# Optimization experiments

Hardware: AMD Instinct MI355X
Metric: run time of the kernel (lower is better)

The kernel has to match this reference:

```python
import jax, jax.numpy as jnp
import numpy as np

B, T, L = 32, 256, 784          # batch, decode steps, context length (H*W)
H, E, V = 512, 256, 8000        # decoder hidden, embedding dim, vocab


def setup_inputs() -> dict:
    key = jax.random.key(0)
    ks = jax.random.split(key, 8)
    s = 0.02
    return {
        "cnn_feats": jax.random.normal(ks[0], (B, L, H), jnp.float32),
        "seq": jax.random.randint(ks[1], (B, T), 0, V),
        "embed_w": jax.random.normal(ks[2], (V, E), jnp.float32) * s,
        "w_ih": jax.random.normal(ks[3], (4 * H, E + H), jnp.float32) * s,
        "w_hh": jax.random.normal(ks[4], (4 * H, H), jnp.float32) * s,
        "w_hm": jax.random.normal(ks[5], (H, H), jnp.float32) * s,
        "w_out": jax.random.normal(ks[6], (H, 2 * H), jnp.float32) * s,
        "w_logit": jax.random.normal(ks[7], (V, H), jnp.float32) * s,
        "b_logit": jnp.zeros((V,), jnp.float32),
    }


def reference(cnn_feats, seq, embed_w, w_ih, w_hh, w_hm, w_out, w_logit, b_logit):
    # embed = Embedding -> ReLU (dropout is identity in eval / p=0)
    xs = jax.nn.relu(embed_w[seq])                      # [B, T, E]
    z = jnp.zeros((B, H), cnn_feats.dtype)

    def step(carry, xt):
        h, c, ctx_out = carry
        # LSTMCell (bias=False), input = concat([xt, prev context_output])
        inp = jnp.concatenate([xt, ctx_out], axis=-1)   # [B, E+H]
        gates = inp @ w_ih.T + h @ w_hh.T               # [B, 4H]
        i, f, g, o = jnp.split(gates, 4, axis=-1)       # torch gate order i,f,g,o
        c = jax.nn.sigmoid(f) * c + jax.nn.sigmoid(i) * jnp.tanh(g)
        h = jax.nn.sigmoid(o) * jnp.tanh(c)
        # dot-product attention over context
        mapped = h @ w_hm.T                             # [B, H]
        attn = jax.nn.softmax(jnp.einsum('blh,bh->bl', cnn_feats, mapped), axis=-1)
        ctx = jnp.einsum('bl,blh->bh', attn, cnn_feats)  # [B, H]
        out = jnp.tanh(jnp.concatenate([ctx, h], axis=-1) @ w_out.T)  # [B, H]
        logp = jax.nn.log_softmax(out @ w_logit.T + b_logit, axis=-1)  # [B, V]
        return (h, c, out), logp

    _, logps = jax.lax.scan(step, (z, z, z), jnp.swapaxes(xs, 0, 1))
    return jnp.swapaxes(logps, 0, 1)                    # [B, T, V]
```

## Files before the change

kernel.cpp:

```cpp
#include <hip/hip_runtime.h>
#include <hip/hip_bf16.h>
#include <stdint.h>

typedef unsigned short u16;
typedef unsigned int u32;
typedef unsigned long long u64;
typedef __attribute__((ext_vector_type(8))) short s16x8;
typedef __attribute__((ext_vector_type(4))) float f32x4;

#define AGT __HIP_MEMORY_SCOPE_AGENT

static __device__ __forceinline__ float bf2f(u16 u){
  unsigned v = ((unsigned)u) << 16; return __builtin_bit_cast(float, v);
}
static __device__ __forceinline__ u16 f2bf(float f){
  unsigned u = __builtin_bit_cast(unsigned, f);
  u += 0x7FFFu + ((u >> 16) & 1u);
  return (u16)(u >> 16);
}
static __device__ __forceinline__ float sigm(float x){ return 1.f / (1.f + __expf(-x)); }

typedef __attribute__((address_space(1))) const u32 gu32;
typedef __attribute__((address_space(3))) u32 lu32;
static __device__ __forceinline__ void gload_lds16(const void* g, void* l){
  __builtin_amdgcn_global_load_lds((gu32*)g, (lu32*)l, 16, 0, 0);
}

static __device__ __forceinline__ u64 tload(const u64* p){
  return __hip_atomic_load(p, __ATOMIC_RELAXED, AGT);
}
static __device__ __forceinline__ void tstore(u64* p, u64 v){
  __hip_atomic_store(p, v, __ATOMIC_RELAXED, AGT);
}
static __device__ __forceinline__ u32 wtag(u64 v){ return (u32)(v >> 32); }
static __device__ __forceinline__ s16x8 pack4(u64 q0, u64 q1, u64 q2, u64 q3){
  u32 a0=(u32)q0, a1=(u32)q1, a2=(u32)q2, a3=(u32)q3;
  s16x8 r = {(short)a0,(short)(a0>>16),(short)a1,(short)(a1>>16),
             (short)a2,(short)(a2>>16),(short)a3,(short)(a3>>16)};
  return r;
}


__global__ __launch_bounds__(256) void k_wfull(const float* __restrict__ wih,
                                               const float* __restrict__ whh,
                                               u16* __restrict__ wf){
  int stride = gridDim.x * blockDim.x;
  for (int i = blockIdx.x * blockDim.x + threadIdx.x; i < 2048 * 1280; i += stride){
    int j = i / 1280, k = i - j * 1280;
    float v = (k < 768) ? wih[j * 768 + k] : whh[j * 512 + (k - 768)];
    wf[i] = f2bf(v);
  }
}

__global__ __launch_bounds__(256) void k_whmt(const float* __restrict__ whm,
                                              u16* __restrict__ wt){
  int stride = gridDim.x * blockDim.x;
  for (int i = blockIdx.x * blockDim.x + threadIdx.x; i < 512 * 512; i += stride){
    int n = i >> 9, k = i & 511;
    wt[i] = f2bf(whm[k * 512 + n]);
  }
}

__global__ __launch_bounds__(256) void k_cvt(const float* __restrict__ s,
                                             u16* __restrict__ d, int n){
  int stride = gridDim.x * blockDim.x * 4;
  for (int i = (blockIdx.x * blockDim.x + threadIdx.x) * 4; i < n; i += stride){
    float4 v = *(const float4*)&s[i];
    d[i + 0] = f2bf(v.x); d[i + 1] = f2bf(v.y);
    d[i + 2] = f2bf(v.z); d[i + 3] = f2bf(v.w);
  }
}

__global__ __launch_bounds__(256) void k_xs(const int* __restrict__ seq,
                                            const float* __restrict__ emb,
                                            u16* __restrict__ xs){
  int stride = gridDim.x * blockDim.x;
  for (int i = blockIdx.x * blockDim.x + threadIdx.x; i < 8192 * 256; i += stride){
    int m = i >> 8, e = i & 255;
    int b = m >> 8, t = m & 255;
    float v = emb[(size_t)seq[m] * 256 + e];
    xs[(size_t)(t * 32 + b) * 256 + e] = f2bf(v > 0.f ? v : 0.f);
  }
}


template<int OUTBF, int HASBIAS, int NG>
__global__ __launch_bounds__(256) void k_gemm(const u16* __restrict__ A,
                                              const u16* __restrict__ Bm,
                                              void* __restrict__ Cout,
                                              const float* __restrict__ bias,
                                              int M, int N, int K){
  __shared__ __align__(16) u16 As[128 * 64];
  __shared__ __align__(16) u16 Bs[128 * 64];
  int tid = threadIdx.x; int w = tid >> 6; int l = tid & 63;
  int m0 = blockIdx.x * 128, n0 = blockIdx.y * 128;
  int wr = w >> 1, wc = w & 1;
  f32x4 acc[4][4];
#pragma unroll
  for (int a = 0; a < 4; a++)
#pragma unroll
    for (int b = 0; b < 4; b++){ f32x4 z = {0.f,0.f,0.f,0.f}; acc[a][b] = z; }
  int rA = m0 + (tid >> 3);
  int rB = n0 + (tid >> 3);
  for (int k0 = 0; k0 < K; k0 += 64){
    __syncthreads();
    int ca = k0 + (tid & 7) * 8;
#pragma unroll
    for (int i = 0; i < 4; i++){
      gload_lds16(&A[(size_t)(rA + i * 32) * K + ca], &As[i * 2048 + w * 512]);
      int rb = rB + i * 32;
      if (NG) rb = (rb < N - 1) ? rb : (N - 1);
      gload_lds16(&Bm[(size_t)rb * K + ca], &Bs[i * 2048 + w * 512]);
    }
    asm volatile("s_waitcnt vmcnt(0)" ::: "memory");
    __syncthreads();
#pragma unroll
    for (int ks = 0; ks < 2; ks++){
      s16x8 av[4], bv[4];
      int ko = ks * 32 + (l >> 4) * 8;
#pragma unroll
      for (int i = 0; i < 4; i++) av[i] = *(const s16x8*)&As[(wr * 64 + i * 16 + (l & 15)) * 64 + ko];
#pragma unroll
      for (int i = 0; i < 4; i++) bv[i] = *(const s16x8*)&Bs[(wc * 64 + i * 16 + (l & 15)) * 64 + ko];
#pragma unroll
      for (int mi = 0; mi < 4; mi++)
#pragma unroll
        for (int ni = 0; ni < 4; ni++)
          acc[mi][ni] = __builtin_amdgcn_mfma_f32_16x16x32_bf16(av[mi], bv[ni], acc[mi][ni], 0, 0, 0);
    }
  }
#pragma unroll
  for (int mi = 0; mi < 4; mi++)
#pragma unroll
    for (int ni = 0; ni < 4; ni++){
      int row = m0 + wr * 64 + mi * 16 + (l >> 4) * 4;
      int col = n0 + wc * 64 + ni * 16 + (l & 15);
      if (NG && col >= N) continue;
#pragma unroll
      for (int r = 0; r < 4; r++){
        float v = acc[mi][ni][r];
        if (HASBIAS) v += bias[col];
        if (OUTBF) ((u16*)Cout)[(size_t)(row + r) * N + col] = f2bf(v);
        else       ((float*)Cout)[(size_t)(row + r) * N + col] = v;
      }
    }
}


static __device__ void gates_role(const u16* __restrict__ WF, const u16* __restrict__ XS,
                                  u64* __restrict__ ZH, u64* __restrict__ ZO,
                                  float* __restrict__ CST, float* __restrict__ SM, int g){
  const int tid = threadIdx.x, w = tid >> 6, l = tid & 63;
  const int ns = g << 4;
  float (*red)[32][64] = (float(*)[32][64])SM;

  s16x8 bx[2][4], bh[4][4], bo[4][4];
#pragma unroll
  for (int ki = 0; ki < 2; ki++){
    int ko = w * 64 + ki * 32 + (l >> 4) * 8;
#pragma unroll
    for (int gi = 0; gi < 4; gi++)
      bx[ki][gi] = *(const s16x8*)&WF[(size_t)(gi * 512 + ns + (l & 15)) * 1280 + ko];
  }
#pragma unroll
  for (int ki = 0; ki < 4; ki++){
    int koh = 768 + w * 128 + ki * 32 + (l >> 4) * 8;
    int koo = 256 + w * 128 + ki * 32 + (l >> 4) * 8;
#pragma unroll
    for (int gi = 0; gi < 4; gi++){
      bh[ki][gi] = *(const s16x8*)&WF[(size_t)(gi * 512 + ns + (l & 15)) * 1280 + koh];
      bo[ki][gi] = *(const s16x8*)&WF[(size_t)(gi * 512 + ns + (l & 15)) * 1280 + koo];
    }
  }

  for (int t = 0; t < 256; ++t){
    const u32 tg = (u32)t;
    const int rp = (t + 1) & 1;
    f32x4 acc[2][4];
#pragma unroll
    for (int a = 0; a < 2; a++)
#pragma unroll
      for (int b = 0; b < 4; b++){ f32x4 z = {0.f,0.f,0.f,0.f}; acc[a][b] = z; }

#pragma unroll
    for (int ki = 0; ki < 2; ki++){
      int ko = w * 64 + ki * 32 + (l >> 4) * 8;
      s16x8 av[2];
#pragma unroll
      for (int mi = 0; mi < 2; mi++)
        av[mi] = *(const s16x8*)&XS[(size_t)(t * 32 + mi * 16 + (l & 15)) * 256 + ko];
#pragma unroll
      for (int mi = 0; mi < 2; mi++)
#pragma unroll
        for (int gi = 0; gi < 4; gi++)
          acc[mi][gi] = __builtin_amdgcn_mfma_f32_16x16x32_bf16(av[mi], bx[ki][gi], acc[mi][gi], 0, 0, 0);
    }
    if (t > 0){
#pragma unroll
      for (int kk = 0; kk < 4; kk++){
        int wb = w * 64 + kk * 16 + ((l >> 4) << 2);
        const u64* p0 = &ZH[(size_t)rp * 8192 + (size_t)(l & 15) * 256 + wb];
        const u64* p1 = &ZH[(size_t)rp * 8192 + (size_t)(16 + (l & 15)) * 256 + wb];
        u64 qa0,qa1,qa2,qa3,qb0,qb1,qb2,qb3; bool ok;
        do {
          qa0=tload(p0); qa1=tload(p0+1); qa2=tload(p0+2); qa3=tload(p0+3);
          qb0=tload(p1); qb1=tload(p1+1); qb2=tload(p1+2); qb3=tload(p1+3);
          ok = (wtag(qa0)==tg)&(wtag(qa1)==tg)&(wtag(qa2)==tg)&(wtag(qa3)==tg)
             & (wtag(qb0)==tg)&(wtag(qb1)==tg)&(wtag(qb2)==tg)&(wtag(qb3)==tg);
          if (!ok) __builtin_amdgcn_s_sleep(1);
        } while (!__all(ok));
        s16x8 av0 = pack4(qa0,qa1,qa2,qa3), av1 = pack4(qb0,qb1,qb2,qb3);
#pragma unroll
        for (int gi = 0; gi < 4; gi++){
          acc[0][gi] = __builtin_amdgcn_mfma_f32_16x16x32_bf16(av0, bh[kk][gi], acc[0][gi], 0, 0, 0);
          acc[1][gi] = __builtin_amdgcn_mfma_f32_16x16x32_bf16(av1, bh[kk][gi], acc[1][gi], 0, 0, 0);
        }
      }
#pragma unroll
      for (int kk = 0; kk < 4; kk++){
        int wb = w * 64 + kk * 16 + ((l >> 4) << 2);
        const u64* p0 = &ZO[(size_t)rp * 8192 + (size_t)(l & 15) * 256 + wb];
        const u64* p1 = &ZO[(size_t)rp * 8192 + (size_t)(16 + (l & 15)) * 256 + wb];
        u64 qa0,qa1,qa2,qa3,qb0,qb1,qb2,qb3; bool ok;
        do {
          qa0=tload(p0); qa1=tload(p0+1); qa2=tload(p0+2); qa3=tload(p0+3);
          qb0=tload(p1); qb1=tload(p1+1); qb2=tload(p1+2); qb3=tload(p1+3);
          ok = (wtag(qa0)==tg)&(wtag(qa1)==tg)&(wtag(qa2)==tg)&(wtag(qa3)==tg)
             & (wtag(qb0)==tg)&(wtag(qb1)==tg)&(wtag(qb2)==tg)&(wtag(qb3)==tg);
          if (!ok) __builtin_amdgcn_s_sleep(1);
        } while (!__all(ok));
        s16x8 av0 = pack4(qa0,qa1,qa2,qa3), av1 = pack4(qb0,qb1,qb2,qb3);
#pragma unroll
        for (int gi = 0; gi < 4; gi++){
          acc[0][gi] = __builtin_amdgcn_mfma_f32_16x16x32_bf16(av0, bo[kk][gi], acc[0][gi], 0, 0, 0);
          acc[1][gi] = __builtin_amdgcn_mfma_f32_16x16x32_bf16(av1, bo[kk][gi], acc[1][gi], 0, 0, 0);
        }
      }
    }
#pragma unroll
    for (int mi = 0; mi < 2; mi++)
#pragma unroll
      for (int gi = 0; gi < 4; gi++)
#pragma unroll
        for (int r = 0; r < 4; r++)
          red[w][mi * 16 + (l >> 4) * 4 + r][gi * 16 + (l & 15)] = acc[mi][gi][r];
    __syncthreads();
    {
      int bi = tid >> 3, j = (tid & 7) * 2;
      float iv0=0,fv0=0,gv0=0,ov0=0, iv1=0,fv1=0,gv1=0,ov1=0;
#pragma unroll
      for (int qq = 0; qq < 4; qq++){
        iv0 += red[qq][bi][j];      fv0 += red[qq][bi][16 + j];
        gv0 += red[qq][bi][32 + j]; ov0 += red[qq][bi][48 + j];
        iv1 += red[qq][bi][j + 1];      fv1 += red[qq][bi][16 + j + 1];
        gv1 += red[qq][bi][32 + j + 1]; ov1 += red[qq][bi][48 + j + 1];
      }
      int n0 = ns + j;
      float c0 = (t > 0) ? CST[bi * 512 + n0]     : 0.f;
      float c1 = (t > 0) ? CST[bi * 512 + n0 + 1] : 0.f;
      float cn0 = sigm(fv0) * c0 + sigm(iv0) * tanhf(gv0);
      float cn1 = sigm(fv1) * c1 + sigm(iv1) * tanhf(gv1);
      float h0 = sigm(ov0) * tanhf(cn0);
      float h1 = sigm(ov1) * tanhf(cn1);
      CST[bi * 512 + n0] = cn0; CST[bi * 512 + n0 + 1] = cn1;
      u32 pk = (u32)f2bf(h0) | ((u32)f2bf(h1) << 16);
      tstore(&ZH[(size_t)(t & 1) * 8192 + (size_t)bi * 256 + g * 8 + (tid & 7)],
             ((u64)(u32)(t + 1) << 32) | pk);
    }
    __syncthreads();
  }
}


static __device__ void attn_role(const u16* __restrict__ CNN2, const u16* __restrict__ CNNB,
                                 const u16* __restrict__ WOUT,
                                 u64* __restrict__ ZH, u64* __restrict__ ZO,
                                 u64* __restrict__ UT, u64* __restrict__ MST,
                                 u16* __restrict__ OALL, float* __restrict__ SM, int q){
  const int tid = threadIdx.x, w = tid >> 6, l = tid & 63;
  const int b = q / 7, ch = q - b * 7;
  const int l0 = ch * 112;
  const int nc = (ch == 6) ? 68 : 74, cs = ch * 74;
  u16*   hsh  = (u16*)SM;
  u16*   pbf  = (u16*)(SM + 256);
  float* sc   = SM + 320;
  float* scp  = SM + 448;
  float* msh  = SM + 896;
  u32*   zsh  = (u32*)(SM + 912);
  float* opart= SM + 1424;

  s16x8 a2[7][4];
  s16x8 vb[8][4];
#pragma unroll
  for (int tile = 0; tile < 7; tile++)
#pragma unroll
    for (int kk = 0; kk < 4; kk++)
      a2[tile][kk] = *(const s16x8*)&CNN2[(size_t)(b * 784 + l0 + tile * 16 + (l & 15)) * 512
                                          + w * 128 + kk * 32 + (l >> 4) * 8];
#pragma unroll
  for (int nt = 0; nt < 8; nt++)
#pragma unroll
    for (int kk = 0; kk < 4; kk++){
      int col = w * 128 + nt * 16 + (l & 15);
#pragma unroll
      for (int j = 0; j < 8; j++){
        int krow = kk * 32 + (l >> 4) * 8 + j;
        vb[nt][kk][j] = (krow < 112)
          ? (short)CNNB[(size_t)(b * 784 + l0 + krow) * 512 + col] : (short)0;
      }
    }

  for (int t = 0; t < 256; ++t){
    const u32 tagp = (u32)(t + 1);
    if (w == 0){
      const u64* hp = &ZH[(size_t)(t & 1) * 8192 + (size_t)b * 256 + l * 4];
      u64 h0,h1,h2,h3; bool ok;
      do {
        h0=tload(hp); h1=tload(hp+1); h2=tload(hp+2); h3=tload(hp+3);
        ok = (wtag(h0)==tagp)&(wtag(h1)==tagp)&(wtag(h2)==tagp)&(wtag(h3)==tagp);
        if (!ok) __builtin_amdgcn_s_sleep(1);
      } while (!__all(ok));
      *(s16x8*)&hsh[l * 8] = pack4(h0,h1,h2,h3);
    }
    __syncthreads();

    f32x4 sac[7];
#pragma unroll
    for (int tile = 0; tile < 7; tile++){ f32x4 z = {0.f,0.f,0.f,0.f}; sac[tile] = z; }
#pragma unroll
    for (int kk = 0; kk < 4; kk++){
      s16x8 bv = *(const s16x8*)&hsh[w * 128 + kk * 32 + (l >> 4) * 8];
#pragma unroll
      for (int tile = 0; tile < 7; tile++)
        sac[tile] = __builtin_amdgcn_mfma_f32_16x16x32_bf16(a2[tile][kk], bv, sac[tile], 0, 0, 0);
    }
    if ((l & 15) == 0){
#pragma unroll
      for (int tile = 0; tile < 7; tile++)
#pragma unroll
        for (int r = 0; r < 4; r++)
          scp[w * 112 + tile * 16 + (l >> 4) * 4 + r] = sac[tile][r];
    }
    __syncthreads();
    if (tid < 112) sc[tid] = scp[tid] + scp[112 + tid] + scp[224 + tid] + scp[336 + tid];
    else if (tid < 128) sc[tid] = -1e30f;
    __syncthreads();
    float m2 = fmaxf(sc[l], sc[l + 64]);
#pragma unroll
    for (int mk = 1; mk < 64; mk <<= 1) m2 = fmaxf(m2, __shfl_xor(m2, mk, 64));
    float M = m2;
    __syncthreads();
    if (tid < 112){ float p = __expf(sc[tid] - M); sc[tid] = p; pbf[tid] = f2bf(p); }
    else if (tid < 128){ sc[tid] = 0.f; pbf[tid] = 0; }
    __syncthreads();
    float s2 = sc[l] + sc[l + 64];
#pragma unroll
    for (int mk = 1; mk < 64; mk <<= 1) s2 += __shfl_xor(s2, mk, 64);
    float S = s2;

    f32x4 uac[8];
#pragma unroll
    for (int nt = 0; nt < 8; nt++){ f32x4 z = {0.f,0.f,0.f,0.f}; uac[nt] = z; }
#pragma unroll
    for (int kk = 0; kk < 4; kk++){
      s16x8 av = *(const s16x8*)&pbf[kk * 32 + (l >> 4) * 8];
#pragma unroll
      for (int nt = 0; nt < 8; nt++)
        uac[nt] = __builtin_amdgcn_mfma_f32_16x16x32_bf16(av, vb[nt][kk], uac[nt], 0, 0, 0);
    }
#pragma unroll
    for (int nt = 0; nt < 8; nt++){
      float o0 = uac[nt][0];
      float o1 = __shfl_xor(o0, 1, 64);
      if (l < 16 && (l & 1) == 0){
        u64 wv = ((u64)tagp << 32) | (u32)f2bf(o0) | ((u32)f2bf(o1) << 16);
        tstore(&UT[((size_t)(b * 7 + ch)) * 256 + w * 64 + nt * 8 + (l >> 1)], wv);
      }
    }
    if (tid == 0){
      tstore(&MST[(b * 7 + ch) * 2 + 0], ((u64)tagp << 32) | __builtin_bit_cast(u32, M));
      tstore(&MST[(b * 7 + ch) * 2 + 1], ((u64)tagp << 32) | __builtin_bit_cast(u32, S));
    }

    if (w == 0){
      const u64* mp_ = &MST[(b * 7) * 2 + ((l < 14) ? l : 0)];
      u64 v; bool ok;
      do {
        v = tload(mp_);
        ok = (wtag(v) == tagp);
        if (!ok) __builtin_amdgcn_s_sleep(1);
      } while (!__all(ok));
      if (l < 14) msh[l] = __builtin_bit_cast(float, (u32)v);
    }
    __syncthreads();
    float Mg = -1e30f;
#pragma unroll
    for (int c = 0; c < 7; c++) Mg = fmaxf(Mg, msh[2 * c]);
    float bet[7]; float Sg = 0.f;
#pragma unroll
    for (int c = 0; c < 7; c++){
      float e = __expf(msh[2 * c] - Mg);
      bet[c] = e; Sg += e * msh[2 * c + 1];
    }
    float inv = 1.f / Sg;
    {
      u64 uw[7]; bool ok;
      do {
#pragma unroll
        for (int c = 0; c < 7; c++) uw[c] = tload(&UT[((size_t)(b * 7 + c)) * 256 + tid]);
        ok = true;
#pragma unroll
        for (int c = 0; c < 7; c++) ok &= (wtag(uw[c]) == tagp);
        if (!ok) __builtin_amdgcn_s_sleep(1);
      } while (!__all(ok));
      float c0 = 0.f, c1 = 0.f;
#pragma unroll
      for (int c = 0; c < 7; c++){
        float bc = bet[c] * inv;
        c0 = fmaf(bc, bf2f((u16)uw[c]), c0);
        c1 = fmaf(bc, bf2f((u16)(uw[c] >> 16)), c1);
      }
      zsh[tid] = (u32)f2bf(c0) | ((u32)f2bf(c1) << 16);
      zsh[256 + tid] = ((u32*)hsh)[tid];
    }
    __syncthreads();

    f32x4 oac[5];
#pragma unroll
    for (int tile = 0; tile < 5; tile++){ f32x4 z = {0.f,0.f,0.f,0.f}; oac[tile] = z; }
#pragma unroll
    for (int kk = 0; kk < 8; kk++){
      int ko = w * 256 + kk * 32 + (l >> 4) * 8;
      s16x8 bv = *(const s16x8*)((const u16*)zsh + ko);
#pragma unroll
      for (int tile = 0; tile < 5; tile++){
        int row = cs + tile * 16 + (l & 15);
        row = (row < 511) ? row : 511;
        s16x8 av = *(const s16x8*)&WOUT[(size_t)row * 1024 + ko];
        oac[tile] = __builtin_amdgcn_mfma_f32_16x16x32_bf16(av, bv, oac[tile], 0, 0, 0);
      }
    }
    if ((l & 15) == 0){
#pragma unroll
      for (int tile = 0; tile < 5; tile++)
#pragma unroll
        for (int r = 0; r < 4; r++)
          opart[w * 80 + tile * 16 + (l >> 4) * 4 + r] = oac[tile][r];
    }
    __syncthreads();
    if (tid < (nc >> 1)){
      int j0 = 2 * tid;
      float v0 = opart[j0]   + opart[80 + j0]   + opart[160 + j0]   + opart[240 + j0];
      float v1 = opart[j0+1] + opart[80 + j0+1] + opart[160 + j0+1] + opart[240 + j0+1];
      u32 pk = (u32)f2bf(tanhf(v0)) | ((u32)f2bf(tanhf(v1)) << 16);
      tstore(&ZO[(size_t)(t & 1) * 8192 + (size_t)b * 256 + (cs >> 1) + tid],
             ((u64)tagp << 32) | pk);
      *(u32*)&OALL[((size_t)(b * 256 + t)) * 512 + cs + j0] = pk;
    }
    __syncthreads();
  }
}


__global__ __launch_bounds__(256, 1) void k_persist(const u16* __restrict__ WF,
                                                    const u16* __restrict__ XS,
                                                    const u16* __restrict__ CNN2,
                                                    const u16* __restrict__ CNNB,
                                                    const u16* __restrict__ WOUT,
                                                    u64* __restrict__ ZH,
                                                    u64* __restrict__ ZO,
                                                    u64* __restrict__ UT,
                                                    u64* __restrict__ MST,
                                                    float* __restrict__ CST,
                                                    u16* __restrict__ OALL){
  __shared__ __align__(16) float SM[8192];
  int gid = blockIdx.x;
  if (gid < 32)
    gates_role(WF, XS, ZH, ZO, CST, SM, gid);
  else
    attn_role(CNN2, CNNB, WOUT, ZH, ZO, UT, MST, OALL, SM, gid - 32);
}


__global__ __launch_bounds__(256) void k_lsm(float* __restrict__ x){
  size_t base = (size_t)blockIdx.x * 8000;
  int tid = threadIdx.x, w = tid >> 6, ln = tid & 63;
  __shared__ float sred[4];
  float m = -1e30f;
  for (int v = tid; v < 8000; v += 256) m = fmaxf(m, x[base + v]);
#pragma unroll
  for (int mk = 1; mk < 64; mk <<= 1) m = fmaxf(m, __shfl_xor(m, mk, 64));
  if (ln == 0) sred[w] = m;
  __syncthreads();
  float M = fmaxf(fmaxf(sred[0], sred[1]), fmaxf(sred[2], sred[3]));
  __syncthreads();
  float s = 0.f;
  for (int v = tid; v < 8000; v += 256) s += __expf(x[base + v] - M);
#pragma unroll
  for (int mk = 1; mk < 64; mk <<= 1) s += __shfl_xor(s, mk, 64);
  if (ln == 0) sred[w] = s;
  __syncthreads();
  float S = sred[0] + sred[1] + sred[2] + sred[3];
  float lz = M + logf(S);
  for (int v = tid; v < 8000; v += 256) x[base + v] -= lz;
}


extern "C" void kernel_launch(void* const* d_in, const int* in_sizes, int n_in,
                              void* d_out, int out_size, void* d_ws, size_t ws_size,
                              hipStream_t stream){
  const float* cnn  = (const float*)d_in[0];
  const int*   seq  = (const int*)d_in[1];
  const float* emb  = (const float*)d_in[2];
  const float* wih  = (const float*)d_in[3];
  const float* whh  = (const float*)d_in[4];
  const float* whm  = (const float*)d_in[5];
  const float* wo   = (const float*)d_in[6];
  const float* wlg  = (const float*)d_in[7];
  const float* blg  = (const float*)d_in[8];

  char* ws = (char*)d_ws;
  u16*   WF     = (u16*)(ws + 0);
  u16*   WHMT   = (u16*)(ws + 5242880);
  u16*   WOUT   = (u16*)(ws + 5767168);
  u16*   WLOGIT = (u16*)(ws + 6815744);
  u16*   CNNBF  = (u16*)(ws + 15007744);
  u16*   CNN2   = (u16*)(ws + 40697856);
  u16*   XS     = (u16*)(ws + 66387968);
  u16*   OALL   = (u16*)(ws + 70582272);
  u64*   ZH     = (u64*)(ws + 78970880);
  u64*   ZO     = (u64*)(ws + 79101952);
  u64*   UT     = (u64*)(ws + 79233024);
  u64*   MST    = (u64*)(ws + 79691776);
  float* CST    = (float*)(ws + 79695360);

  float* OUT = (float*)d_out;

  (void)hipMemsetAsync(ws + 78970880, 0, 724480, stream);
  k_wfull<<<512, 256, 0, stream>>>(wih, whh, WF);
  k_whmt<<<128, 256, 0, stream>>>(whm, WHMT);
  k_cvt<<<512, 256, 0, stream>>>(wo, WOUT, 512 * 1024);
  k_cvt<<<2048, 256, 0, stream>>>(wlg, WLOGIT, 8000 * 512);
  k_cvt<<<2048, 256, 0, stream>>>(cnn, CNNBF, 25088 * 512);
  k_xs<<<2048, 256, 0, stream>>>(seq, emb, XS);

  {
    dim3 g(196, 4);
    k_gemm<1, 0, 0><<<g, 256, 0, stream>>>(CNNBF, WHMT, CNN2, nullptr, 25088, 512, 512);
  }

  k_persist<<<256, 256, 0, stream>>>(WF, XS, CNN2, CNNBF, WOUT, ZH, ZO, UT, MST, CST, OALL);

  {
    dim3 g(64, 63);
    k_gemm<0, 1, 1><<<g, 256, 0, stream>>>(OALL, WLOGIT, OUT, blg, 8192, 8000, 512);
  }
  k_lsm<<<8192, 256, 0, stream>>>(OUT);
}
```

Measured before the change: 3.497 ms.

## Parallelize attention polling, drop barriers, and use one-pass online log-softmax

```diff
diff --git a/kernel.cpp b/kernel.cpp
--- a/kernel.cpp
+++ b/kernel.cpp
@@ -288,6 +288,7 @@
   float* msh  = SM + 896;
   u32*   zsh  = (u32*)(SM + 912);
   float* opart= SM + 1424;
+  float* pexp = SM + 1744;
 
   s16x8 a2[7][4];
   s16x8 vb[8][4];
@@ -312,15 +313,15 @@
 
   for (int t = 0; t < 256; ++t){
     const u32 tagp = (u32)(t + 1);
-    if (w == 0){
-      const u64* hp = &ZH[(size_t)(t & 1) * 8192 + (size_t)b * 256 + l * 4];
-      u64 h0,h1,h2,h3; bool ok;
+    {
+      const u64* hp = &ZH[(size_t)(t & 1) * 8192 + (size_t)b * 256 + tid];
+      u64 hw; bool ok;
       do {
-        h0=tload(hp); h1=tload(hp+1); h2=tload(hp+2); h3=tload(hp+3);
-        ok = (wtag(h0)==tagp)&(wtag(h1)==tagp)&(wtag(h2)==tagp)&(wtag(h3)==tagp);
+        hw = tload(hp);
+        ok = (wtag(hw) == tagp);
         if (!ok) __builtin_amdgcn_s_sleep(1);
       } while (!__all(ok));
-      *(s16x8*)&hsh[l * 8] = pack4(h0,h1,h2,h3);
+      ((u32*)hsh)[tid] = (u32)hw;
     }
     __syncthreads();
 
@@ -349,11 +350,10 @@
 #pragma unroll
     for (int mk = 1; mk < 64; mk <<= 1) m2 = fmaxf(m2, __shfl_xor(m2, mk, 64));
     float M = m2;
-    __syncthreads();
-    if (tid < 112){ float p = __expf(sc[tid] - M); sc[tid] = p; pbf[tid] = f2bf(p); }
-    else if (tid < 128){ sc[tid] = 0.f; pbf[tid] = 0; }
-    __syncthreads();
-    float s2 = sc[l] + sc[l + 64];
+    if (tid < 112){ float p = __expf(sc[tid] - M); pexp[tid] = p; pbf[tid] = f2bf(p); }
+    else if (tid < 128){ pexp[tid] = 0.f; pbf[tid] = 0; }
+    __syncthreads();
+    float s2 = pexp[l] + pexp[l + 64];
 #pragma unroll
     for (int mk = 1; mk < 64; mk <<= 1) s2 += __shfl_xor(s2, mk, 64);
     float S = s2;
@@ -382,16 +382,23 @@
       tstore(&MST[(b * 7 + ch) * 2 + 1], ((u64)tagp << 32) | __builtin_bit_cast(u32, S));
     }
 
-    if (w == 0){
-      const u64* mp_ = &MST[(b * 7) * 2 + ((l < 14) ? l : 0)];
-      u64 v; bool ok;
+    u64 uw[7]; u64 msv = 0;
+    {
+      bool ok;
       do {
-        v = tload(mp_);
-        ok = (wtag(v) == tagp);
+#pragma unroll
+        for (int c = 0; c < 7; c++) uw[c] = tload(&UT[((size_t)(b * 7 + c)) * 256 + tid]);
+        ok = true;
+#pragma unroll
+        for (int c = 0; c < 7; c++) ok &= (wtag(uw[c]) == tagp);
+        if (w == 0){
+          msv = tload(&MST[b * 14 + ((l < 14) ? l : 0)]);
+          ok &= (wtag(msv) == tagp);
+        }
         if (!ok) __builtin_amdgcn_s_sleep(1);
       } while (!__all(ok));
-      if (l < 14) msh[l] = __builtin_bit_cast(float, (u32)v);
-    }
+    }
+    if (w == 0 && l < 14) msh[l] = __builtin_bit_cast(float, (u32)msv);
     __syncthreads();
     float Mg = -1e30f;
 #pragma unroll
@@ -404,15 +411,6 @@
     }
     float inv = 1.f / Sg;
     {
-      u64 uw[7]; bool ok;
-      do {
-#pragma unroll
-        for (int c = 0; c < 7; c++) uw[c] = tload(&UT[((size_t)(b * 7 + c)) * 256 + tid]);
-        ok = true;
-#pragma unroll
-        for (int c = 0; c < 7; c++) ok &= (wtag(uw[c]) == tagp);
-        if (!ok) __builtin_amdgcn_s_sleep(1);
-      } while (!__all(ok));
       float c0 = 0.f, c1 = 0.f;
 #pragma unroll
       for (int c = 0; c < 7; c++){
@@ -485,24 +483,41 @@
 __global__ __launch_bounds__(256) void k_lsm(float* __restrict__ x){
   size_t base = (size_t)blockIdx.x * 8000;
   int tid = threadIdx.x, w = tid >> 6, ln = tid & 63;
-  __shared__ float sred[4];
-  float m = -1e30f;
-  for (int v = tid; v < 8000; v += 256) m = fmaxf(m, x[base + v]);
-#pragma unroll
-  for (int mk = 1; mk < 64; mk <<= 1) m = fmaxf(m, __shfl_xor(m, mk, 64));
-  if (ln == 0) sred[w] = m;
+  __shared__ float sm_[4], ss_[4];
+  const float4* xv = (const float4*)(x + base);
+  float m = -1e30f, s = 0.f;
+  for (int v = tid; v < 2000; v += 256){
+    float4 f = xv[v];
+    float mm = fmaxf(fmaxf(f.x, f.y), fmaxf(f.z, f.w));
+    float ss = __expf(f.x-mm)+__expf(f.y-mm)+__expf(f.z-mm)+__expf(f.w-mm);
+    float nm = fmaxf(m, mm);
+    s = s * __expf(m - nm) + ss * __expf(mm - nm);
+    m = nm;
+  }
+#pragma unroll
+  for (int mk = 1; mk < 64; mk <<= 1){
+    float mo = __shfl_xor(m, mk, 64), so = __shfl_xor(s, mk, 64);
+    float nm = fmaxf(m, mo);
+    s = s * __expf(m - nm) + so * __expf(mo - nm);
+    m = nm;
+  }
+  if (ln == 0){ sm_[w] = m; ss_[w] = s; }
   __syncthreads();
-  float M = fmaxf(fmaxf(sred[0], sred[1]), fmaxf(sred[2], sred[3]));
-  __syncthreads();
-  float s = 0.f;
-  for (int v = tid; v < 8000; v += 256) s += __expf(x[base + v] - M);
-#pragma unroll
-  for (int mk = 1; mk < 64; mk <<= 1) s += __shfl_xor(s, mk, 64);
-  if (ln == 0) sred[w] = s;
-  __syncthreads();
-  float S = sred[0] + sred[1] + sred[2] + sred[3];
+  float M = -1e30f, S = 0.f;
+#pragma unroll
+  for (int q2 = 0; q2 < 4; q2++){
+    float mo = sm_[q2], so = ss_[q2];
+    float nm = fmaxf(M, mo);
+    S = S * __expf(M - nm) + so * __expf(mo - nm);
+    M = nm;
+  }
   float lz = M + logf(S);
-  for (int v = tid; v < 8000; v += 256) x[base + v] -= lz;
+  float4* xw = (float4*)(x + base);
+  for (int v = tid; v < 2000; v += 256){
+    float4 f = xw[v];
+    f.x -= lz; f.y -= lz; f.z -= lz; f.w -= lz;
+    xw[v] = f;
+  }
 }
 
 
```

New measurement: 3.346 ms. 1.05x faster.
